# Optimization experiments

Hardware: AMD Instinct MI355X
Metric: run time of the kernel (lower is better)

## Reference

```python
import jax, jax.numpy as jnp
import numpy as np

N = 50000        # nodes
E = 800000       # edges (avg degree 16)
F_IN = 11        # raw node features
HID = 128        # hidden_dim
HEADS = 4
C = HID // HEADS # per-head channels = 32
L = 4            # num_layers
NEG_SLOPE = 0.2  # PyG GATv2 default


def setup_inputs() -> dict:
    key = jax.random.key(0)
    ks = jax.random.split(key, 10)
    s = 0.1
    node_features = jax.random.normal(ks[0], (N, F_IN), jnp.float32)
    edge_index = jax.random.randint(ks[1], (2, E), 0, N, dtype=jnp.int32)
    W_emb = jax.random.normal(ks[2], (HID, F_IN), jnp.float32) * s
    b_emb = jnp.zeros((HID,), jnp.float32)
    Wl = jax.random.normal(ks[3], (L, HID, HID), jnp.float32) * s
    bl = jnp.zeros((L, HID), jnp.float32)
    Wr = jax.random.normal(ks[4], (L, HID, HID), jnp.float32) * s
    br = jnp.zeros((L, HID), jnp.float32)
    att = jax.random.normal(ks[5], (L, HEADS, C), jnp.float32) * s
    bias = jnp.zeros((L, HID), jnp.float32)
    return {
        "node_features": node_features, "edge_index": edge_index, "num_nodes": N,
        "W_emb": W_emb, "b_emb": b_emb, "Wl": Wl, "bl": bl,
        "Wr": Wr, "br": br, "att": att, "bias": bias,
    }


def _gatv2_layer(x, src, dst, Wl, bl, Wr, br, att, bias):
    """PyG GATv2Conv (concat=True, share_weights=False), dropout off."""
    n = x.shape[0]
    xl = (x @ Wl.T + bl).reshape(n, HEADS, C)  # source transform
    xr = (x @ Wr.T + br).reshape(n, HEADS, C)  # target transform
    e = jax.nn.leaky_relu(xl[src] + xr[dst], NEG_SLOPE)       # [E,H,C]
    logits = jnp.einsum('ehc,hc->eh', e, att)                 # [E,H]
    # segment softmax over incoming edges per destination node
    m = jax.ops.segment_max(logits, dst, num_segments=n)      # [N,H]
    m = jnp.where(jnp.isfinite(m), m, jnp.zeros_like(m))      # empty segments
    p = jnp.exp(logits - m[dst])                              # [E,H]
    denom = jax.ops.segment_sum(p, dst, num_segments=n)       # [N,H]
    alpha = p / denom[dst]
    out = jax.ops.segment_sum(alpha[:, :, None] * xl[src], dst, num_segments=n)
    return out.reshape(n, HID) + bias


def reference(node_features, edge_index, num_nodes, W_emb, b_emb, Wl, bl, Wr, br, att, bias):
    src, dst = edge_index[0], edge_index[1]
    x = jax.nn.relu(node_features @ W_emb.T + b_emb)
    for i in range(L):  # BatchNorms exist in the torch module but are never applied
        x_res = x
        x = _gatv2_layer(x, src, dst, Wl[i], bl[i], Wr[i], br[i], att[i], bias[i])
        x = jax.nn.relu(x)
        if i > 0:
            x = x + x_res
    graph_mean = jnp.mean(x, axis=0)
    graph_max = jnp.max(x, axis=0)
    graph_embedding = jnp.concatenate([graph_mean, graph_max], axis=-1)  # [2*HID]
    return graph_embedding, x
```

## Files before the change

### kernel.cpp

```cpp
#include <hip/hip_runtime.h>
#include <math.h>

#define HID 128
#define HEADS 4
#define NEG_SLOPE 0.2f
#define R1B 1024
#define BCAP 8192
#define PB 6144
#define ACHUNK 4096

typedef float f32x4 __attribute__((ext_vector_type(4)));
typedef _Float16 f16x8 __attribute__((ext_vector_type(8)));
typedef _Float16 f16x4 __attribute__((ext_vector_type(4)));
typedef _Float16 f16x2 __attribute__((ext_vector_type(2)));

#if defined(__has_builtin)
#if __has_builtin(__builtin_amdgcn_fdot2)
#define HAVE_FDOT2 1
#endif
#endif


__global__ __launch_bounds__(256) void k_zero_int(int* p, int n) {
    int i = blockIdx.x * blockDim.x + threadIdx.x;
    if (i < n) p[i] = 0;
}

__global__ __launch_bounds__(256) void k_binA(const int* __restrict__ src, const int* __restrict__ dst,
                                              int E, int* __restrict__ gcnt, int* __restrict__ arena) {
    __shared__ int lh[256];
    __shared__ int lbase[256];
    __shared__ unsigned short lrank[ACHUNK];
    const int tid = threadIdx.x;
    lh[tid] = 0;
    __syncthreads();
    const int e0 = blockIdx.x * ACHUNK;
    #pragma unroll
    for (int i = 0; i < ACHUNK / 256; i++) {
        int e = e0 + i * 256 + tid;
        if (e < E) {
            int b = dst[e] >> 8;
            lrank[i * 256 + tid] = (unsigned short)atomicAdd(&lh[b], 1);
        }
    }
    __syncthreads();
    if (lh[tid] > 0) lbase[tid] = atomicAdd(&gcnt[tid], lh[tid]);
    __syncthreads();
    #pragma unroll
    for (int i = 0; i < ACHUNK / 256; i++) {
        int e = e0 + i * 256 + tid;
        if (e < E) {
            int d = dst[e];
            int b = d >> 8;
            arena[b * BCAP + lbase[b] + lrank[i * 256 + tid]] = (src[e] << 8) | (d & 255);
        }
    }
}

__global__ __launch_bounds__(256) void k_scan_bk(const int* __restrict__ gcnt, int nbk,
                                                 int* __restrict__ bstart, int* __restrict__ rowptr,
                                                 int N, int E) {
    __shared__ int buf[256];
    int tid = threadIdx.x;
    int v = (tid < nbk) ? gcnt[tid] : 0;
    buf[tid] = v;
    __syncthreads();
    for (int off = 1; off < 256; off <<= 1) {
        int t = (tid >= off) ? buf[tid - off] : 0;
        __syncthreads();
        buf[tid] += t;
        __syncthreads();
    }
    bstart[tid] = buf[tid] - v;
    if (tid == 0) rowptr[N] = E;
}

__global__ __launch_bounds__(256) void k_binB(const int* __restrict__ arena, const int* __restrict__ gcnt,
                                              const int* __restrict__ bstart, int N,
                                              int* __restrict__ rowptr, int* __restrict__ csr_off) {
    __shared__ int ncnt[256];
    __shared__ int sbuf[256];
    __shared__ int nstart[256];
    __shared__ int stage[PB];
    __shared__ unsigned short rk[BCAP];
    const int b = blockIdx.x, tid = threadIdx.x;
    const int cnt = gcnt[b];
    const int seg = bstart[b];
    ncnt[tid] = 0;
    __syncthreads();
    for (int k = tid; k < cnt; k += 256) {
        int v = arena[b * BCAP + k];
        rk[k] = (unsigned short)atomicAdd(&ncnt[v & 255], 1);
    }
    __syncthreads();
    int c = ncnt[tid];
    sbuf[tid] = c;
    __syncthreads();
    for (int off = 1; off < 256; off <<= 1) {
        int t = (tid >= off) ? sbuf[tid - off] : 0;
        __syncthreads();
        sbuf[tid] += t;
        __syncthreads();
    }
    int myStart = sbuf[tid] - c;
    nstart[tid] = myStart;
    int n = b * 256 + tid;
    if (n < N) rowptr[n] = seg + myStart;
    __syncthreads();
    for (int k = tid; k < cnt; k += 256) {
        int v = arena[b * BCAP + k];
        int pos = nstart[v & 255] + rk[k];
        int val = v & 0xFFFFFF00;
        if (pos < PB) stage[pos] = val;
        else          csr_off[seg + pos] = val;
    }
    __syncthreads();
    int lim = min(cnt, PB);
    for (int k = tid; k < lim; k += 256) csr_off[seg + k] = stage[k];
}


__device__ inline f16x2 absh2(f16x2 v) {
    unsigned u = __builtin_bit_cast(unsigned, v) & 0x7FFF7FFFu;
    return __builtin_bit_cast(f16x2, u);
}

__global__ __launch_bounds__(256) void k_tof16(const float* __restrict__ a, const float* __restrict__ b,
                                               _Float16* __restrict__ oa, _Float16* __restrict__ ob, int n) {
    const float* x = blockIdx.y ? b : a;
    _Float16*    o = blockIdx.y ? ob : oa;
    int base = (blockIdx.x * 256 + threadIdx.x) * 4;
    if (base >= n) return;
    float4 v = *(const float4*)(x + base);
    f16x4 h = {(_Float16)v.x, (_Float16)v.y, (_Float16)v.z, (_Float16)v.w};
    *(f16x4*)(o + base) = h;
}


__global__ __launch_bounds__(512) void k_linear_mfma(
        const _Float16* __restrict__ xh,
        const _Float16* __restrict__ WfL, const _Float16* __restrict__ WfR,
        const float* __restrict__ bl, const float* __restrict__ br,
        _Float16* __restrict__ xlh, _Float16* __restrict__ xrh, int N) {
    __shared__ _Float16 lds[16384];
    const int t   = threadIdx.x;
    const int mat = blockIdx.y;
    const _Float16* W = mat ? WfR : WfL;

    for (int g = t; g < 2048; g += 512) {
        int r = g >> 4, cc = g & 15;
        int dsto = r * 128 + ((cc ^ (r & 7)) << 3);
        *(float4*)&lds[dsto] = *(const float4*)(W + g * 8);
    }
    __syncthreads();

    const int wave = t >> 6;
    const int lane = t & 63;
    const int l16  = lane & 15;
    const int quad = lane >> 4;
    const int n0   = blockIdx.x * 256 + wave * 32;

    int arow0 = n0 + l16;
    int arow1 = n0 + 16 + l16;
    if (arow0 >= N) arow0 = N - 1;
    if (arow1 >= N) arow1 = N - 1;

    f32x4 acc[2][8];
    #pragma unroll
    for (int u = 0; u < 2; u++)
        #pragma unroll
        for (int s = 0; s < 8; s++) acc[u][s] = (f32x4){0.f, 0.f, 0.f, 0.f};

    #pragma unroll
    for (int k0 = 0; k0 < HID; k0 += 32) {
        f16x8 a0 = *(const f16x8*)(xh + arow0 * HID + k0 + quad * 8);
        f16x8 a1 = *(const f16x8*)(xh + arow1 * HID + k0 + quad * 8);
        const int cc = (k0 >> 3) + quad;
        #pragma unroll
        for (int s = 0; s < 8; s++) {
            const int row = s * 16 + l16;
            const int off = row * 128 + ((cc ^ (l16 & 7)) << 3);
            f16x8 b = *(const f16x8*)&lds[off];
            acc[0][s] = __builtin_amdgcn_mfma_f32_16x16x32_f16(a0, b, acc[0][s], 0, 0, 0);
            acc[1][s] = __builtin_amdgcn_mfma_f32_16x16x32_f16(a1, b, acc[1][s], 0, 0, 0);
        }
    }

    const float* bias = mat ? br : bl;
    _Float16* dst = mat ? xrh : xlh;
    #pragma unroll
    for (int s = 0; s < 8; s++) {
        int col = s * 16 + l16;
        float bv = bias[col];
        #pragma unroll
        for (int u = 0; u < 2; u++) {
            #pragma unroll
            for (int r = 0; r < 4; r++) {
                int node = n0 + u * 16 + quad * 4 + r;
                if (node < N) dst[(size_t)node * HID + col] = (_Float16)(acc[u][s][r] + bv);
            }
        }
    }
}


__global__ __launch_bounds__(256) void k_attn(const _Float16* __restrict__ xlh, const _Float16* __restrict__ xrh,
                                              const int* __restrict__ rowptr, const int* __restrict__ csr_off,
                                              const float* __restrict__ att, const float* __restrict__ bias,
                                              const _Float16* __restrict__ xres, _Float16* __restrict__ outx,
                                              float* __restrict__ out,
                                              int add_res, int want_half, int N) {
    const int wave = threadIdx.x >> 6;
    const int lane = threadIdx.x & 63;
    const int strm = lane >> 4;
    const int l16  = lane & 15;
    const int n = blockIdx.x * 4 + wave;
    if (n >= N) return;

    const float4 aA = *(const float4*)(att + 8 * l16);
    const float4 aB = *(const float4*)(att + 8 * l16 + 4);
    const f16x2 a0 = (f16x2){(_Float16)aA.x, (_Float16)aA.y};
    const f16x2 a1 = (f16x2){(_Float16)aA.z, (_Float16)aA.w};
    const f16x2 a2 = (f16x2){(_Float16)aB.x, (_Float16)aB.y};
    const f16x2 a3 = (f16x2){(_Float16)aB.z, (_Float16)aB.w};
    const f16x8 xrv = *(const f16x8*)(xrh + (size_t)n * HID + 8 * l16);
    const f16x2 xr0 = __builtin_shufflevector(xrv, xrv, 0, 1);
    const f16x2 xr1 = __builtin_shufflevector(xrv, xrv, 2, 3);
    const f16x2 xr2 = __builtin_shufflevector(xrv, xrv, 4, 5);
    const f16x2 xr3 = __builtin_shufflevector(xrv, xrv, 6, 7);
    const f16x2 k06 = (f16x2){(_Float16)0.6f, (_Float16)0.6f};
    const f16x2 k04 = (f16x2){(_Float16)0.4f, (_Float16)0.4f};
    const int s0 = rowptr[n], s1 = rowptr[n + 1];

    float den = 0.f;
    f16x2 acc16[4];
    #pragma unroll
    for (int q = 0; q < 4; q++) acc16[q] = (f16x2){(_Float16)0.f, (_Float16)0.f};

    const char* xlb = (const char*)xlh + l16 * 16;

    int j = s0 + strm;
    if (j < s1) {
        const int last = s1 - 1;
        f16x8 p0 = *(const f16x8*)(xlb + csr_off[min(j,     last)]);
        f16x8 p1 = *(const f16x8*)(xlb + csr_off[min(j + 4, last)]);
        int   o2 = csr_off[min(j + 8, last)];
        while (j < s1) {
            f16x8 cur = p0;
            p0 = p1;
            p1 = *(const f16x8*)(xlb + o2);
            o2 = csr_off[min(j + 12, last)];

            f16x2 c0 = __builtin_shufflevector(cur, cur, 0, 1);
            f16x2 c1 = __builtin_shufflevector(cur, cur, 2, 3);
            f16x2 c2 = __builtin_shufflevector(cur, cur, 4, 5);
            f16x2 c3 = __builtin_shufflevector(cur, cur, 6, 7);
            f16x2 u0 = c0 + xr0, u1 = c1 + xr1, u2 = c2 + xr2, u3 = c3 + xr3;
            f16x2 l0 = u0 * k06 + absh2(u0) * k04;
            f16x2 l1 = u1 * k06 + absh2(u1) * k04;
            f16x2 l2 = u2 * k06 + absh2(u2) * k04;
            f16x2 l3 = u3 * k06 + absh2(u3) * k04;
#ifdef HAVE_FDOT2
            float p = __builtin_amdgcn_fdot2(l0, a0, 0.f, false);
            p = __builtin_amdgcn_fdot2(l1, a1, p, false);
            p = __builtin_amdgcn_fdot2(l2, a2, p, false);
            p = __builtin_amdgcn_fdot2(l3, a3, p, false);
#else
            float p = (float)l0[0] * (float)a0[0] + (float)l0[1] * (float)a0[1]
                    + (float)l1[0] * (float)a1[0] + (float)l1[1] * (float)a1[1]
                    + (float)l2[0] * (float)a2[0] + (float)l2[1] * (float)a2[1]
                    + (float)l3[0] * (float)a3[0] + (float)l3[1] * (float)a3[1];
#endif
            p += __shfl_xor(p, 1);
            p += __shfl_xor(p, 2);
            float w = __expf(p);
            den += w;
            _Float16 wh = (_Float16)w;
            f16x2 wp = (f16x2){wh, wh};
            acc16[0] += wp * c0;
            acc16[1] += wp * c1;
            acc16[2] += wp * c2;
            acc16[3] += wp * c3;
            j += 4;
        }
    }

    float acc[8];
    #pragma unroll
    for (int q = 0; q < 4; q++) {
        acc[2 * q]     = (float)acc16[q][0];
        acc[2 * q + 1] = (float)acc16[q][1];
    }

    den += __shfl_xor(den, 16);
    den += __shfl_xor(den, 32);
    #pragma unroll
    for (int q = 0; q < 8; q++) {
        acc[q] += __shfl_xor(acc[q], 16);
        acc[q] += __shfl_xor(acc[q], 32);
    }

    if (strm == 0) {
        float4 bA = *(const float4*)(bias + 8 * l16);
        float4 bB = *(const float4*)(bias + 8 * l16 + 4);
        float b[8] = {bA.x, bA.y, bA.z, bA.w, bB.x, bB.y, bB.z, bB.w};
        float inv = (den > 0.f) ? 1.f / den : 0.f;
        float v[8];
        #pragma unroll
        for (int q = 0; q < 8; q++) v[q] = fmaxf(acc[q] * inv + b[q], 0.f);
        if (add_res) {
            f16x8 r = *(const f16x8*)(xres + (size_t)n * HID + 8 * l16);
            #pragma unroll
            for (int q = 0; q < 8; q++) v[q] += (float)r[q];
        }
        if (want_half) {
            f16x8 h;
            #pragma unroll
            for (int q = 0; q < 8; q++) h[q] = (_Float16)v[q];
            *(f16x8*)(outx + (size_t)n * HID + 8 * l16) = h;
        } else {
            *(float4*)(out + (size_t)n * HID + 8 * l16)     = make_float4(v[0], v[1], v[2], v[3]);
            *(float4*)(out + (size_t)n * HID + 8 * l16 + 4) = make_float4(v[4], v[5], v[6], v[7]);
        }
    }
}


__global__ __launch_bounds__(128) void k_embed(const float* __restrict__ nf, const float* __restrict__ W,
                                               const float* __restrict__ b,
                                               _Float16* __restrict__ xh, int N) {
    __shared__ float f[11];
    int n = blockIdx.x;
    int h = threadIdx.x;
    if (h < 11) f[h] = nf[(size_t)n * 11 + h];
    __syncthreads();
    float acc = b[h];
    #pragma unroll
    for (int k = 0; k < 11; k++) acc += f[k] * W[h * 11 + k];
    xh[(size_t)n * HID + h] = (_Float16)fmaxf(acc, 0.f);
}


__global__ __launch_bounds__(256) void k_reduce1(const float* __restrict__ x, int N,
                                                 float* __restrict__ psum, float* __restrict__ pmax) {
    __shared__ float ls[8][HID];
    __shared__ float lm[8][HID];
    const int c4 = (threadIdx.x & 31) << 2;
    const int rl = threadIdx.x >> 5;
    const int per = (N + gridDim.x - 1) / gridDim.x;
    const int n0 = blockIdx.x * per, n1 = min(N, n0 + per);
    float4 s = make_float4(0.f, 0.f, 0.f, 0.f);
    float4 m = make_float4(-INFINITY, -INFINITY, -INFINITY, -INFINITY);
    for (int n = n0 + rl; n < n1; n += 8) {
        float4 v = *(const float4*)(x + (size_t)n * HID + c4);
        s.x += v.x; s.y += v.y; s.z += v.z; s.w += v.w;
        m.x = fmaxf(m.x, v.x); m.y = fmaxf(m.y, v.y);
        m.z = fmaxf(m.z, v.z); m.w = fmaxf(m.w, v.w);
    }
    *(float4*)&ls[rl][c4] = s;
    *(float4*)&lm[rl][c4] = m;
    __syncthreads();
    if (rl < 4) {
        float4 a = *(float4*)&ls[rl][c4], bq = *(float4*)&ls[rl + 4][c4];
        a.x += bq.x; a.y += bq.y; a.z += bq.z; a.w += bq.w;
        *(float4*)&ls[rl][c4] = a;
        float4 am = *(float4*)&lm[rl][c4], bm = *(float4*)&lm[rl + 4][c4];
        am.x = fmaxf(am.x, bm.x); am.y = fmaxf(am.y, bm.y);
        am.z = fmaxf(am.z, bm.z); am.w = fmaxf(am.w, bm.w);
        *(float4*)&lm[rl][c4] = am;
    }
    __syncthreads();
    if (rl < 2) {
        float4 a = *(float4*)&ls[rl][c4], bq = *(float4*)&ls[rl + 2][c4];
        a.x += bq.x; a.y += bq.y; a.z += bq.z; a.w += bq.w;
        *(float4*)&ls[rl][c4] = a;
        float4 am = *(float4*)&lm[rl][c4], bm = *(float4*)&lm[rl + 2][c4];
        am.x = fmaxf(am.x, bm.x); am.y = fmaxf(am.y, bm.y);
        am.z = fmaxf(am.z, bm.z); am.w = fmaxf(am.w, bm.w);
        *(float4*)&lm[rl][c4] = am;
    }
    __syncthreads();
    if (rl == 0) {
        float4 a = *(float4*)&ls[0][c4], bq = *(float4*)&ls[1][c4];
        a.x += bq.x; a.y += bq.y; a.z += bq.z; a.w += bq.w;
        *(float4*)(psum + (size_t)blockIdx.x * HID + c4) = a;
        float4 am = *(float4*)&lm[0][c4], bm = *(float4*)&lm[1][c4];
        am.x = fmaxf(am.x, bm.x); am.y = fmaxf(am.y, bm.y);
        am.z = fmaxf(am.z, bm.z); am.w = fmaxf(am.w, bm.w);
        *(float4*)(pmax + (size_t)blockIdx.x * HID + c4) = am;
    }
}

__global__ __launch_bounds__(1024) void k_reduce2(const float* __restrict__ psum, const float* __restrict__ pmax,
                                                  int nb, float* __restrict__ out, float invN) {
    __shared__ float ss[8][HID];
    __shared__ float sm[8][HID];
    int h = threadIdx.x & 127;
    int c = threadIdx.x >> 7;
    int per = nb >> 3;
    float s = 0.f, m = -INFINITY;
    for (int b = c * per; b < (c + 1) * per; b++) {
        s += psum[b * HID + h];
        m = fmaxf(m, pmax[b * HID + h]);
    }
    ss[c][h] = s; sm[c][h] = m;
    __syncthreads();
    if (c < 4) { ss[c][h] += ss[c + 4][h]; sm[c][h] = fmaxf(sm[c][h], sm[c + 4][h]); }
    __syncthreads();
    if (c < 2) { ss[c][h] += ss[c + 2][h]; sm[c][h] = fmaxf(sm[c][h], sm[c + 2][h]); }
    __syncthreads();
    if (c == 0) {
        out[h] = (ss[0][h] + ss[1][h]) * invN;
        out[HID + h] = fmaxf(sm[0][h], sm[1][h]);
    }
}


extern "C" void kernel_launch(void* const* d_in, const int* in_sizes, int n_in,
                              void* d_out, int out_size, void* d_ws, size_t ws_size,
                              hipStream_t stream) {
    const float* nf    = (const float*)d_in[0];
    const int*   ei    = (const int*)d_in[1];
    const float* W_emb = (const float*)d_in[3];
    const float* b_emb = (const float*)d_in[4];
    const float* Wl    = (const float*)d_in[5];
    const float* bl    = (const float*)d_in[6];
    const float* Wr    = (const float*)d_in[7];
    const float* br    = (const float*)d_in[8];
    const float* att   = (const float*)d_in[9];
    const float* bias  = (const float*)d_in[10];

    const int N = in_sizes[0] / 11;
    const int E = in_sizes[1] / 2;
    const int* src = ei;
    const int* dst = ei + E;

    float* out  = (float*)d_out;
    float* xout = out + 2 * HID;

    char* w = (char*)d_ws;
    _Float16* xlh  = (_Float16*)w; w += (size_t)N * HID * 2;
    _Float16* xrh  = (_Float16*)w; w += (size_t)N * HID * 2;
    _Float16* xA   = (_Float16*)w; w += (size_t)N * HID * 2;
    _Float16* xB   = (_Float16*)w; w += (size_t)N * HID * 2;
    _Float16* WfL  = (_Float16*)w; w += (size_t)4 * HID * HID * 2;
    _Float16* WfR  = (_Float16*)w; w += (size_t)4 * HID * HID * 2;
    int*   gcnt    = (int*)w;   w += (size_t)256 * 4;
    int*   bstart  = (int*)w;   w += (size_t)256 * 4;
    int*   rowptr  = (int*)w;   w += (size_t)(N + 1) * 4;
    int*   arena   = (int*)w;   w += (size_t)256 * BCAP * 4;
    int*   csr_off = (int*)w;   w += (size_t)E * 4;
    float* psum    = (float*)w; w += (size_t)R1B * HID * 4;
    float* pmax    = (float*)w; w += (size_t)R1B * HID * 4;

    const int nbk = (N + 255) >> 8;
    const int nW = 4 * HID * HID;

    dim3 tg((nW / 4 + 255) / 256, 2);
    k_tof16<<<tg, 256, 0, stream>>>(Wl, Wr, WfL, WfR, nW);

    k_zero_int<<<1, 256, 0, stream>>>(gcnt, 256);
    k_binA<<<(E + ACHUNK - 1) / ACHUNK, 256, 0, stream>>>(src, dst, E, gcnt, arena);
    k_scan_bk<<<1, 256, 0, stream>>>(gcnt, nbk, bstart, rowptr, N, E);
    k_binB<<<nbk, 256, 0, stream>>>(arena, gcnt, bstart, N, rowptr, csr_off);

    k_embed<<<N, 128, 0, stream>>>(nf, W_emb, b_emb, xA, N);

    dim3 lgrid((N + 255) / 256, 2);
    for (int i = 0; i < 4; i++) {
        const _Float16* xin = (i & 1) ? xB : xA;
        _Float16* xo        = (i & 1) ? xA : xB;
        k_linear_mfma<<<lgrid, 512, 0, stream>>>(xin,
                                                 WfL + (size_t)i * HID * HID, WfR + (size_t)i * HID * HID,
                                                 bl + i * HID, br + i * HID, xlh, xrh, N);
        k_attn<<<(N + 3) / 4, 256, 0, stream>>>(xlh, xrh, rowptr, csr_off,
                                                att + i * HEADS * 32, bias + i * HID,
                                                xin, xo, xout,
                                                i > 0 ? 1 : 0, i < 3 ? 1 : 0, N);
    }

    k_reduce1<<<R1B, 256, 0, stream>>>(xout, N, psum, pmax);
    k_reduce2<<<1, 1024, 0, stream>>>(psum, pmax, R1B, out, 1.0f / N);
}
```

Measured before the change: 426.1 us.

## Deepen attention gather prefetch, simplify leaky ReLU, halve linear block size

The attention loop now keeps four neighbour feature rows in flight instead of two, prefetching the offset five steps ahead, so more gather latency can be hidden. The leaky ReLU becomes a single elementwise max(u, 0.2u) when the builtin is available, replacing the abs-based formula. The MFMA linear kernel moves from 512-thread blocks covering 256 rows to 256-thread blocks covering 128 rows, doubling the block count and the per-block weight staging into LDS. The deeper prefetch costs extra registers, which may lower occupancy in the attention kernel.

Result: no change. 427.5 us (+0.3%).

```diff
diff --git a/kernel.cpp b/kernel.cpp
--- a/kernel.cpp
+++ b/kernel.cpp
@@ -17,6 +17,9 @@
 #if defined(__has_builtin)
 #if __has_builtin(__builtin_amdgcn_fdot2)
 #define HAVE_FDOT2 1
+#endif
+#if __has_builtin(__builtin_elementwise_max)
+#define HAVE_EMAX 1
 #endif
 #endif
 
@@ -124,6 +127,13 @@
     unsigned u = __builtin_bit_cast(unsigned, v) & 0x7FFF7FFFu;
     return __builtin_bit_cast(f16x2, u);
 }
+__device__ inline f16x2 leaky2(f16x2 u, f16x2 k02, f16x2 k06, f16x2 k04) {
+#ifdef HAVE_EMAX
+    return __builtin_elementwise_max(u, u * k02);
+#else
+    return u * k06 + absh2(u) * k04;
+#endif
+}
 
 __global__ __launch_bounds__(256) void k_tof16(const float* __restrict__ a, const float* __restrict__ b,
                                                _Float16* __restrict__ oa, _Float16* __restrict__ ob, int n) {
@@ -137,7 +147,7 @@
 }
 
 
-__global__ __launch_bounds__(512) void k_linear_mfma(
+__global__ __launch_bounds__(256) void k_linear_mfma(
         const _Float16* __restrict__ xh,
         const _Float16* __restrict__ WfL, const _Float16* __restrict__ WfR,
         const float* __restrict__ bl, const float* __restrict__ br,
@@ -147,7 +157,7 @@
     const int mat = blockIdx.y;
     const _Float16* W = mat ? WfR : WfL;
 
-    for (int g = t; g < 2048; g += 512) {
+    for (int g = t; g < 2048; g += 256) {
         int r = g >> 4, cc = g & 15;
         int dsto = r * 128 + ((cc ^ (r & 7)) << 3);
         *(float4*)&lds[dsto] = *(const float4*)(W + g * 8);
@@ -158,7 +168,7 @@
     const int lane = t & 63;
     const int l16  = lane & 15;
     const int quad = lane >> 4;
-    const int n0   = blockIdx.x * 256 + wave * 32;
+    const int n0   = blockIdx.x * 128 + wave * 32;
 
     int arow0 = n0 + l16;
     int arow1 = n0 + 16 + l16;
@@ -228,6 +238,7 @@
     const f16x2 xr1 = __builtin_shufflevector(xrv, xrv, 2, 3);
     const f16x2 xr2 = __builtin_shufflevector(xrv, xrv, 4, 5);
     const f16x2 xr3 = __builtin_shufflevector(xrv, xrv, 6, 7);
+    const f16x2 k02 = (f16x2){(_Float16)0.2f, (_Float16)0.2f};
     const f16x2 k06 = (f16x2){(_Float16)0.6f, (_Float16)0.6f};
     const f16x2 k04 = (f16x2){(_Float16)0.4f, (_Float16)0.4f};
     const int s0 = rowptr[n], s1 = rowptr[n + 1];
@@ -242,24 +253,25 @@
     int j = s0 + strm;
     if (j < s1) {
         const int last = s1 - 1;
-        f16x8 p0 = *(const f16x8*)(xlb + csr_off[min(j,     last)]);
-        f16x8 p1 = *(const f16x8*)(xlb + csr_off[min(j + 4, last)]);
-        int   o2 = csr_off[min(j + 8, last)];
+        f16x8 p0 = *(const f16x8*)(xlb + csr_off[min(j,      last)]);
+        f16x8 p1 = *(const f16x8*)(xlb + csr_off[min(j + 4,  last)]);
+        f16x8 p2 = *(const f16x8*)(xlb + csr_off[min(j + 8,  last)]);
+        f16x8 p3 = *(const f16x8*)(xlb + csr_off[min(j + 12, last)]);
+        int   o4 = csr_off[min(j + 16, last)];
         while (j < s1) {
             f16x8 cur = p0;
-            p0 = p1;
-            p1 = *(const f16x8*)(xlb + o2);
-            o2 = csr_off[min(j + 12, last)];
+            p0 = p1; p1 = p2; p2 = p3;
+            p3 = *(const f16x8*)(xlb + o4);
+            o4 = csr_off[min(j + 20, last)];
 
             f16x2 c0 = __builtin_shufflevector(cur, cur, 0, 1);
             f16x2 c1 = __builtin_shufflevector(cur, cur, 2, 3);
             f16x2 c2 = __builtin_shufflevector(cur, cur, 4, 5);
             f16x2 c3 = __builtin_shufflevector(cur, cur, 6, 7);
-            f16x2 u0 = c0 + xr0, u1 = c1 + xr1, u2 = c2 + xr2, u3 = c3 + xr3;
-            f16x2 l0 = u0 * k06 + absh2(u0) * k04;
-            f16x2 l1 = u1 * k06 + absh2(u1) * k04;
-            f16x2 l2 = u2 * k06 + absh2(u2) * k04;
-            f16x2 l3 = u3 * k06 + absh2(u3) * k04;
+            f16x2 l0 = leaky2(c0 + xr0, k02, k06, k04);
+            f16x2 l1 = leaky2(c1 + xr1, k02, k06, k04);
+            f16x2 l2 = leaky2(c2 + xr2, k02, k06, k04);
+            f16x2 l3 = leaky2(c3 + xr3, k02, k06, k04);
 #ifdef HAVE_FDOT2
             float p = __builtin_amdgcn_fdot2(l0, a0, 0.f, false);
             p = __builtin_amdgcn_fdot2(l1, a1, p, false);
@@ -466,11 +478,11 @@
 
     k_embed<<<N, 128, 0, stream>>>(nf, W_emb, b_emb, xA, N);
 
-    dim3 lgrid((N + 255) / 256, 2);
+    dim3 lgrid((N + 127) / 128, 2);
     for (int i = 0; i < 4; i++) {
         const _Float16* xin = (i & 1) ? xB : xA;
         _Float16* xo        = (i & 1) ? xA : xB;
-        k_linear_mfma<<<lgrid, 512, 0, stream>>>(xin,
+        k_linear_mfma<<<lgrid, 256, 0, stream>>>(xin,
                                                  WfL + (size_t)i * HID * HID, WfR + (size_t)i * HID * HID,
                                                  bl + i * HID, br + i * HID, xlh, xrh, N);
         k_attn<<<(N + 3) / 4, 256, 0, stream>>>(xlh, xrh, rowptr, csr_off,
```
